# Kernel tuning notes

Hardware: AMD Instinct MI355X
Metric: run time of the kernel (lower is better)

Reference implementation:

```python
import jax, jax.numpy as jnp
import numpy as np

TEMPERATURE = 0.1
EPS = 1e-8


def setup_inputs() -> dict:
    key = jax.random.key(0)
    k1, k2 = jax.random.split(key)
    features = jax.random.normal(k1, (1024, 256, 16, 8), dtype=jnp.float32)
    labels = jax.random.randint(k2, (1024,), 0, 64, dtype=jnp.int64)
    return {"features": features, "labels": labels}


def reference(features, labels):
    B = features.shape[0]
    f = features.reshape(B, -1)
    norm = jnp.clip(jnp.linalg.norm(f, axis=1, keepdims=True), EPS)
    f = f / norm
    # matcher modeled as cosine-similarity gram matrix (opaque TransMatcher out of scope)
    scores = (f @ f.T) / TEMPERATURE  # [B, B]

    same = labels[:, None] == labels[None, :]
    eye = jnp.eye(B, dtype=bool)
    pos = same & ~eye  # positives excluding self
    neg = ~same & ~eye  # negatives excluding self

    # shared max over pos ∪ neg = all off-diagonal entries per row (matches original)
    row_max = jnp.max(jnp.where(eye, -jnp.inf, scores), axis=1, keepdims=True)
    e = jnp.exp(scores - row_max)  # [B, B]
    pos_sum = jnp.sum(jnp.where(pos, e, 0.0), axis=1)
    neg_sum = jnp.sum(jnp.where(neg, e, 0.0), axis=1)

    valid = jnp.any(pos, axis=1) & jnp.any(neg, axis=1)
    safe_pos = jnp.where(valid, pos_sum, 1.0)
    safe_neg = jnp.where(valid, neg_sum, 1.0)
    # loss_i = neg_term - pos_term; shared max cancels
    loss_i = jnp.where(valid, jnp.log(safe_neg) - jnp.log(safe_pos), 0.0)

    total = jnp.sum(valid.astype(jnp.float32))
    loss = jnp.where(total > 0, jnp.sum(loss_i) / jnp.maximum(total, 1.0), 0.0)

    max_pos = jnp.max(jnp.where(pos, scores, -jnp.inf), axis=1)
    max_neg = jnp.max(jnp.where(neg, scores, -jnp.inf), axis=1)
    correct = jnp.sum((valid & (max_pos > max_neg)).astype(jnp.float32))
    accuracy = jnp.where(total > 0, correct / jnp.maximum(total, 1.0), 0.5)
    return loss, accuracy
```

## Files before the change

### kernel.cpp

```cpp
#include <hip/hip_runtime.h>
#include <hip/hip_bf16.h>
#include <stdint.h>

#define BSZ 1024
#define KF 32768
#define SPLITK 32
#define KPER (KF / SPLITK)
#define BKB 128
#define TEMP_INV 10.0f

typedef float f32x4 __attribute__((ext_vector_type(4)));
typedef int v8i __attribute__((ext_vector_type(8)));

__device__ __forceinline__ void async_copy16(const void* g, void* l) {
    __builtin_amdgcn_global_load_lds(
        (const __attribute__((address_space(1))) void*)g,
        (__attribute__((address_space(3))) void*)l, 16, 0, 0);
}

__device__ __forceinline__ unsigned short f2bf_bits(float x) {
    union { float f; uint32_t u; } t; t.f = x;
    uint32_t r = t.u + 0x7FFFu + ((t.u >> 16) & 1u);
    return (unsigned short)(r >> 16);
}
__device__ __forceinline__ float bf2f(unsigned short b) {
    union { uint32_t u; float f; } t; t.u = ((uint32_t)b) << 16; return t.f;
}

__device__ __forceinline__ float waveSum(float v) {
    for (int o = 32; o > 0; o >>= 1) v += __shfl_down(v, o);
    return v;
}
__device__ __forceinline__ float waveMax(float v) {
    for (int o = 32; o > 0; o >>= 1) v = fmaxf(v, __shfl_down(v, o));
    return v;
}
__device__ __forceinline__ float blockSum(float v, float* red, int tid) {
    v = waveSum(v);
    __syncthreads();
    if ((tid & 63) == 0) red[tid >> 6] = v;
    __syncthreads();
    return red[0] + red[1] + red[2] + red[3];
}
__device__ __forceinline__ float blockMax(float v, float* red, int tid) {
    v = waveMax(v);
    __syncthreads();
    if ((tid & 63) == 0) red[tid >> 6] = v;
    __syncthreads();
    return fmaxf(fmaxf(red[0], red[1]), fmaxf(red[2], red[3]));
}

__global__ __launch_bounds__(256) void k_norm_convert(
    const float* __restrict__ f, unsigned char* __restrict__ f8,
    float* __restrict__ inv_norm) {
    int row = blockIdx.x, tid = threadIdx.x;
    const float4* src = (const float4*)(f + (size_t)row * KF);
    int4* dst = (int4*)(f8 + (size_t)row * KF);
    float ss = 0.f;
    for (int o = 0; o < 8; ++o) {
        int base4 = o * 1024 + tid * 4;
        int4 pk;
        int* pkp = &pk.x;
#pragma unroll
        for (int q = 0; q < 4; ++q) {
            float4 v = src[base4 + q];
            ss += v.x * v.x + v.y * v.y + v.z * v.z + v.w * v.w;
            int wd = __builtin_amdgcn_cvt_pk_fp8_f32(v.x, v.y, 0, false);
            wd = __builtin_amdgcn_cvt_pk_fp8_f32(v.z, v.w, wd, true);
            pkp[q] = wd;
        }
        dst[o * 256 + tid] = pk;
    }
    __shared__ float red[4];
    float tot = blockSum(ss, red, tid);
    if (tid == 0) inv_norm[row] = 1.0f / fmaxf(sqrtf(tot), 1e-8f);
}

__global__ __launch_bounds__(256) void k_gemm(
    const unsigned char* __restrict__ f8, unsigned short* __restrict__ partials) {
    __shared__ unsigned char Alds[128 * BKB];
    __shared__ unsigned char Blds[128 * BKB];
    int tid = threadIdx.x;

    int t = blockIdx.x;
    int bi = 0, accu = 0;
    while (accu + bi + 1 <= t) { accu += bi + 1; ++bi; }
    int bj = t - accu;
    int row0 = bi * 128, col0 = bj * 128;
    int p = blockIdx.y;
    size_t kbase = (size_t)p * KPER;

    const unsigned char* Ag = f8 + (size_t)row0 * KF;
    const unsigned char* Bg = f8 + (size_t)col0 * KF;
    int lane = tid & 63, w = tid >> 6;
    int wrow = (w >> 1) * 64, wcol = (w & 1) * 64;
    int mrow = lane & 15, quad = lane >> 4;

    int r_st[4], g_st[4];
#pragma unroll
    for (int c = 0; c < 4; ++c) {
        int idx = c * 256 + tid;
        r_st[c] = idx >> 3;
        g_st[c] = (idx & 7) ^ (r_st[c] & 7);
    }

    f32x4 acc[4][4] = {};

    for (int kt = 0; kt < KPER / BKB; ++kt) {
        size_t k0 = kbase + (size_t)kt * BKB;
        __syncthreads();
#pragma unroll
        for (int c = 0; c < 4; ++c) {
            int idx = c * 256 + tid;
            async_copy16(Ag + (size_t)r_st[c] * KF + k0 + g_st[c] * 16, &Alds[idx * 16]);
            async_copy16(Bg + (size_t)r_st[c] * KF + k0 + g_st[c] * 16, &Blds[idx * 16]);
        }
        __syncthreads();
        v8i a8[4], b8[4];
#pragma unroll
        for (int mi = 0; mi < 4; ++mi) {
            int rA = wrow + mi * 16 + mrow;
            int4 lo = *(const int4*)&Alds[rA * BKB + ((quad * 2)     ^ (rA & 7)) * 16];
            int4 hi = *(const int4*)&Alds[rA * BKB + ((quad * 2 + 1) ^ (rA & 7)) * 16];
            a8[mi] = (v8i){lo.x, lo.y, lo.z, lo.w, hi.x, hi.y, hi.z, hi.w};
        }
#pragma unroll
        for (int ni = 0; ni < 4; ++ni) {
            int rB = wcol + ni * 16 + mrow;
            int4 lo = *(const int4*)&Blds[rB * BKB + ((quad * 2)     ^ (rB & 7)) * 16];
            int4 hi = *(const int4*)&Blds[rB * BKB + ((quad * 2 + 1) ^ (rB & 7)) * 16];
            b8[ni] = (v8i){lo.x, lo.y, lo.z, lo.w, hi.x, hi.y, hi.z, hi.w};
        }
#pragma unroll
        for (int mi = 0; mi < 4; ++mi)
#pragma unroll
            for (int ni = 0; ni < 4; ++ni)
                acc[mi][ni] = __builtin_amdgcn_mfma_scale_f32_16x16x128_f8f6f4(
                    a8[mi], b8[ni], acc[mi][ni],
                    0, 0,
                    0, 0x7F7F7F7F,
                    0, 0x7F7F7F7F);
    }

    unsigned short* outp = partials + (size_t)p * BSZ * BSZ;
#pragma unroll
    for (int mi = 0; mi < 4; ++mi)
#pragma unroll
        for (int ni = 0; ni < 4; ++ni)
#pragma unroll
            for (int r = 0; r < 4; ++r) {
                int row = row0 + wrow + mi * 16 + quad * 4 + r;
                int col = col0 + wcol + ni * 16 + mrow;
                outp[(size_t)row * BSZ + col] = f2bf_bits(acc[mi][ni][r]);
            }
    if (bi != bj) {
#pragma unroll
        for (int mi = 0; mi < 4; ++mi)
#pragma unroll
            for (int ni = 0; ni < 4; ++ni) {
                int rowm = col0 + wcol + ni * 16 + mrow;
                int colm = row0 + wrow + mi * 16 + quad * 4;
                ushort4 v;
                v.x = f2bf_bits(acc[mi][ni][0]);
                v.y = f2bf_bits(acc[mi][ni][1]);
                v.z = f2bf_bits(acc[mi][ni][2]);
                v.w = f2bf_bits(acc[mi][ni][3]);
                *(ushort4*)&outp[(size_t)rowm * BSZ + colm] = v;
            }
    }
}

__global__ __launch_bounds__(256) void k_loss_rows(
    const unsigned short* __restrict__ partials, const float* __restrict__ inv_norm,
    const int* __restrict__ labels, float* __restrict__ rloss,
    float* __restrict__ rvalid, float* __restrict__ rcorr) {
    int i = blockIdx.x, tid = threadIdx.x;
    __shared__ float srow[BSZ];
    __shared__ int slab[BSZ];
    __shared__ float red[4];
    for (int c = 0; c < 4; ++c) slab[c * 256 + tid] = labels[c * 256 + tid];
    float inv_i = inv_norm[i];

    int j4 = tid * 4;
    float sx = 0.f, sy = 0.f, sz = 0.f, sw = 0.f;
#pragma unroll
    for (int p2 = 0; p2 < SPLITK; ++p2) {
        ushort4 v = *(const ushort4*)&partials[(size_t)p2 * BSZ * BSZ + (size_t)i * BSZ + j4];
        sx += bf2f(v.x); sy += bf2f(v.y); sz += bf2f(v.z); sw += bf2f(v.w);
    }
    float4 invj = *(const float4*)&inv_norm[j4];
    srow[j4 + 0] = sx * inv_i * invj.x * TEMP_INV;
    srow[j4 + 1] = sy * inv_i * invj.y * TEMP_INV;
    srow[j4 + 2] = sz * inv_i * invj.z * TEMP_INV;
    srow[j4 + 3] = sw * inv_i * invj.w * TEMP_INV;
    __syncthreads();

    int lab_i = slab[i];
    float lm = -3.0e38f;
    for (int c = 0; c < 4; ++c) {
        int j = c * 256 + tid;
        if (j != i) lm = fmaxf(lm, srow[j]);
    }
    float rowmax = blockMax(lm, red, tid);

    float pos_sum = 0.f, neg_sum = 0.f, mp = -3.0e38f, mn = -3.0e38f;
    for (int c = 0; c < 4; ++c) {
        int j = c * 256 + tid;
        if (j == i) continue;
        float s = srow[j];
        float e = expf(s - rowmax);
        if (slab[j] == lab_i) { pos_sum += e; mp = fmaxf(mp, s); }
        else                  { neg_sum += e; mn = fmaxf(mn, s); }
    }
    float ps = blockSum(pos_sum, red, tid);
    float ns = blockSum(neg_sum, red, tid);
    float mpa = blockMax(mp, red, tid);
    float mna = blockMax(mn, red, tid);
    if (tid == 0) {
        bool valid = (mpa > -1.0e37f) && (mna > -1.0e37f);
        rloss[i]  = valid ? (logf(ns) - logf(ps)) : 0.f;
        rvalid[i] = valid ? 1.f : 0.f;
        rcorr[i]  = (valid && (mpa > mna)) ? 1.f : 0.f;
    }
}

__global__ __launch_bounds__(256) void k_final(
    const float* __restrict__ rloss, const float* __restrict__ rvalid,
    const float* __restrict__ rcorr, float* __restrict__ out) {
    __shared__ float red[4];
    int tid = threadIdx.x;
    float sl = 0.f, sv = 0.f, sc = 0.f;
    for (int c = 0; c < 4; ++c) {
        int j = c * 256 + tid;
        sl += rloss[j]; sv += rvalid[j]; sc += rcorr[j];
    }
    sl = blockSum(sl, red, tid);
    sv = blockSum(sv, red, tid);
    sc = blockSum(sc, red, tid);
    if (tid == 0) {
        out[0] = (sv > 0.f) ? sl / fmaxf(sv, 1.f) : 0.f;
        out[1] = (sv > 0.f) ? sc / fmaxf(sv, 1.f) : 0.5f;
    }
}

extern "C" void kernel_launch(void* const* d_in, const int* in_sizes, int n_in,
                              void* d_out, int out_size, void* d_ws, size_t ws_size,
                              hipStream_t stream) {
    const float* feats = (const float*)d_in[0];
    const int* labels = (const int*)d_in[1];
    float* out = (float*)d_out;
    char* ws = (char*)d_ws;

    unsigned char* f8        = (unsigned char*)ws;
    unsigned short* partials = (unsigned short*)(ws + (size_t)32 * 1024 * 1024);
    float* inv_norm          = (float*)(ws + (size_t)96 * 1024 * 1024);
    float* rloss             = inv_norm + BSZ;
    float* rvalid            = rloss + BSZ;
    float* rcorr             = rvalid + BSZ;

    k_norm_convert<<<BSZ, 256, 0, stream>>>(feats, f8, inv_norm);
    k_gemm<<<dim3(36, SPLITK), 256, 0, stream>>>(f8, partials);
    k_loss_rows<<<BSZ, 256, 0, stream>>>(partials, inv_norm, labels, rloss, rvalid, rcorr);
    k_final<<<1, 256, 0, stream>>>(rloss, rvalid, rcorr, out);
}
```

Baseline: 263.7 us.

## Store split-K partials in fp8, use fixed exp shift, fuse final reduction via atomics

Split-K partial sums of the Gram matrix are now stored as fp8 instead of bf16, which halves the partial buffer traffic written by the GEMM and read by the loss kernel. The per-row max pass is removed by using a constant shift of 10 (the maximum possible cosine score over the temperature), and the exp call becomes the fast intrinsic. The final reduction kernel is folded into the loss kernel through global atomics and a last-block ticket. In exchange, fp8 partials lose a lot of precision across 32 accumulated slices, the fixed shift could underflow for rows whose scores are all far below 10, and float atomics make the summation order nondeterministic.

```diff
diff --git a/kernel.cpp b/kernel.cpp
--- a/kernel.cpp
+++ b/kernel.cpp
@@ -18,15 +18,6 @@
         (__attribute__((address_space(3))) void*)l, 16, 0, 0);
 }
 
-__device__ __forceinline__ unsigned short f2bf_bits(float x) {
-    union { float f; uint32_t u; } t; t.f = x;
-    uint32_t r = t.u + 0x7FFFu + ((t.u >> 16) & 1u);
-    return (unsigned short)(r >> 16);
-}
-__device__ __forceinline__ float bf2f(unsigned short b) {
-    union { uint32_t u; float f; } t; t.u = ((uint32_t)b) << 16; return t.f;
-}
-
 __device__ __forceinline__ float waveSum(float v) {
     for (int o = 32; o > 0; o >>= 1) v += __shfl_down(v, o);
     return v;
@@ -52,8 +43,9 @@
 
 __global__ __launch_bounds__(256) void k_norm_convert(
     const float* __restrict__ f, unsigned char* __restrict__ f8,
-    float* __restrict__ inv_norm) {
+    float* __restrict__ inv_norm, float* __restrict__ gaccum) {
     int row = blockIdx.x, tid = threadIdx.x;
+    if (row == 0 && tid < 4) gaccum[tid] = 0.f;
     const float4* src = (const float4*)(f + (size_t)row * KF);
     int4* dst = (int4*)(f8 + (size_t)row * KF);
     float ss = 0.f;
@@ -77,7 +69,7 @@
 }
 
 __global__ __launch_bounds__(256) void k_gemm(
-    const unsigned char* __restrict__ f8, unsigned short* __restrict__ partials) {
+    const unsigned char* __restrict__ f8, unsigned char* __restrict__ partials) {
     __shared__ unsigned char Alds[128 * BKB];
     __shared__ unsigned char Blds[128 * BKB];
     int tid = threadIdx.x;
@@ -142,7 +134,7 @@
                     0, 0x7F7F7F7F);
     }
 
-    unsigned short* outp = partials + (size_t)p * BSZ * BSZ;
+    unsigned char* outp = partials + (size_t)p * BSZ * BSZ;
 #pragma unroll
     for (int mi = 0; mi < 4; ++mi)
 #pragma unroll
@@ -151,7 +143,9 @@
             for (int r = 0; r < 4; ++r) {
                 int row = row0 + wrow + mi * 16 + quad * 4 + r;
                 int col = col0 + wcol + ni * 16 + mrow;
-                outp[(size_t)row * BSZ + col] = f2bf_bits(acc[mi][ni][r]);
+                int b = __builtin_amdgcn_cvt_pk_fp8_f32(
+                            acc[mi][ni][r], acc[mi][ni][r], 0, false);
+                outp[(size_t)row * BSZ + col] = (unsigned char)(b & 0xFF);
             }
     if (bi != bj) {
 #pragma unroll
@@ -160,24 +154,23 @@
             for (int ni = 0; ni < 4; ++ni) {
                 int rowm = col0 + wcol + ni * 16 + mrow;
                 int colm = row0 + wrow + mi * 16 + quad * 4;
-                ushort4 v;
-                v.x = f2bf_bits(acc[mi][ni][0]);
-                v.y = f2bf_bits(acc[mi][ni][1]);
-                v.z = f2bf_bits(acc[mi][ni][2]);
-                v.w = f2bf_bits(acc[mi][ni][3]);
-                *(ushort4*)&outp[(size_t)rowm * BSZ + colm] = v;
+                int pk = __builtin_amdgcn_cvt_pk_fp8_f32(
+                             acc[mi][ni][0], acc[mi][ni][1], 0, false);
+                pk = __builtin_amdgcn_cvt_pk_fp8_f32(
+                         acc[mi][ni][2], acc[mi][ni][3], pk, true);
+                *(int*)&outp[(size_t)rowm * BSZ + colm] = pk;
             }
     }
 }
 
 __global__ __launch_bounds__(256) void k_loss_rows(
-    const unsigned short* __restrict__ partials, const float* __restrict__ inv_norm,
-    const int* __restrict__ labels, float* __restrict__ rloss,
-    float* __restrict__ rvalid, float* __restrict__ rcorr) {
+    const unsigned char* __restrict__ partials, const float* __restrict__ inv_norm,
+    const int* __restrict__ labels, float* __restrict__ gaccum,
+    float* __restrict__ out) {
     int i = blockIdx.x, tid = threadIdx.x;
-    __shared__ float srow[BSZ];
     __shared__ int slab[BSZ];
     __shared__ float red[4];
+    __shared__ int s_ticket;
     for (int c = 0; c < 4; ++c) slab[c * 256 + tid] = labels[c * 256 + tid];
     float inv_i = inv_norm[i];
 
@@ -185,30 +178,28 @@
     float sx = 0.f, sy = 0.f, sz = 0.f, sw = 0.f;
 #pragma unroll
     for (int p2 = 0; p2 < SPLITK; ++p2) {
-        ushort4 v = *(const ushort4*)&partials[(size_t)p2 * BSZ * BSZ + (size_t)i * BSZ + j4];
-        sx += bf2f(v.x); sy += bf2f(v.y); sz += bf2f(v.z); sw += bf2f(v.w);
+        int v = *(const int*)&partials[(size_t)p2 * BSZ * BSZ + (size_t)i * BSZ + j4];
+        sx += __builtin_amdgcn_cvt_f32_fp8(v, 0);
+        sy += __builtin_amdgcn_cvt_f32_fp8(v, 1);
+        sz += __builtin_amdgcn_cvt_f32_fp8(v, 2);
+        sw += __builtin_amdgcn_cvt_f32_fp8(v, 3);
     }
     float4 invj = *(const float4*)&inv_norm[j4];
-    srow[j4 + 0] = sx * inv_i * invj.x * TEMP_INV;
-    srow[j4 + 1] = sy * inv_i * invj.y * TEMP_INV;
-    srow[j4 + 2] = sz * inv_i * invj.z * TEMP_INV;
-    srow[j4 + 3] = sw * inv_i * invj.w * TEMP_INV;
+    float s4[4];
+    s4[0] = sx * inv_i * invj.x * TEMP_INV;
+    s4[1] = sy * inv_i * invj.y * TEMP_INV;
+    s4[2] = sz * inv_i * invj.z * TEMP_INV;
+    s4[3] = sw * inv_i * invj.w * TEMP_INV;
     __syncthreads();
 
     int lab_i = slab[i];
-    float lm = -3.0e38f;
-    for (int c = 0; c < 4; ++c) {
-        int j = c * 256 + tid;
-        if (j != i) lm = fmaxf(lm, srow[j]);
-    }
-    float rowmax = blockMax(lm, red, tid);
-
     float pos_sum = 0.f, neg_sum = 0.f, mp = -3.0e38f, mn = -3.0e38f;
-    for (int c = 0; c < 4; ++c) {
-        int j = c * 256 + tid;
+#pragma unroll
+    for (int q = 0; q < 4; ++q) {
+        int j = j4 + q;
         if (j == i) continue;
-        float s = srow[j];
-        float e = expf(s - rowmax);
+        float s = s4[q];
+        float e = __expf(s - 10.0f);
         if (slab[j] == lab_i) { pos_sum += e; mp = fmaxf(mp, s); }
         else                  { neg_sum += e; mn = fmaxf(mn, s); }
     }
@@ -216,28 +207,21 @@
     float ns = blockSum(neg_sum, red, tid);
     float mpa = blockMax(mp, red, tid);
     float mna = blockMax(mn, red, tid);
+
     if (tid == 0) {
         bool valid = (mpa > -1.0e37f) && (mna > -1.0e37f);
-        rloss[i]  = valid ? (logf(ns) - logf(ps)) : 0.f;
-        rvalid[i] = valid ? 1.f : 0.f;
-        rcorr[i]  = (valid && (mpa > mna)) ? 1.f : 0.f;
-    }
-}
-
-__global__ __launch_bounds__(256) void k_final(
-    const float* __restrict__ rloss, const float* __restrict__ rvalid,
-    const float* __restrict__ rcorr, float* __restrict__ out) {
-    __shared__ float red[4];
-    int tid = threadIdx.x;
-    float sl = 0.f, sv = 0.f, sc = 0.f;
-    for (int c = 0; c < 4; ++c) {
-        int j = c * 256 + tid;
-        sl += rloss[j]; sv += rvalid[j]; sc += rcorr[j];
-    }
-    sl = blockSum(sl, red, tid);
-    sv = blockSum(sv, red, tid);
-    sc = blockSum(sc, red, tid);
-    if (tid == 0) {
+        float li = valid ? (logf(ns) - logf(ps)) : 0.f;
+        atomicAdd(&gaccum[0], li);
+        atomicAdd(&gaccum[1], valid ? 1.f : 0.f);
+        atomicAdd(&gaccum[2], (valid && (mpa > mna)) ? 1.f : 0.f);
+        __threadfence();
+        s_ticket = atomicAdd((int*)&gaccum[3], 1);
+    }
+    __syncthreads();
+    if (s_ticket == BSZ - 1 && tid == 0) {
+        float sl = atomicAdd(&gaccum[0], 0.f);
+        float sv = atomicAdd(&gaccum[1], 0.f);
+        float sc = atomicAdd(&gaccum[2], 0.f);
         out[0] = (sv > 0.f) ? sl / fmaxf(sv, 1.f) : 0.f;
         out[1] = (sv > 0.f) ? sc / fmaxf(sv, 1.f) : 0.5f;
     }
@@ -251,15 +235,12 @@
     float* out = (float*)d_out;
     char* ws = (char*)d_ws;
 
-    unsigned char* f8        = (unsigned char*)ws;
-    unsigned short* partials = (unsigned short*)(ws + (size_t)32 * 1024 * 1024);
-    float* inv_norm          = (float*)(ws + (size_t)96 * 1024 * 1024);
-    float* rloss             = inv_norm + BSZ;
-    float* rvalid            = rloss + BSZ;
-    float* rcorr             = rvalid + BSZ;
-
-    k_norm_convert<<<BSZ, 256, 0, stream>>>(feats, f8, inv_norm);
+    unsigned char* f8       = (unsigned char*)ws;
+    unsigned char* partials = (unsigned char*)(ws + (size_t)32 * 1024 * 1024);
+    float* inv_norm         = (float*)(ws + (size_t)64 * 1024 * 1024);
+    float* gaccum           = inv_norm + BSZ;
+
+    k_norm_convert<<<BSZ, 256, 0, stream>>>(feats, f8, inv_norm, gaccum);
     k_gemm<<<dim3(36, SPLITK), 256, 0, stream>>>(f8, partials);
-    k_loss_rows<<<BSZ, 256, 0, stream>>>(partials, inv_norm, labels, rloss, rvalid, rcorr);
-    k_final<<<1, 256, 0, stream>>>(rloss, rvalid, rcorr, out);
-}
+    k_loss_rows<<<BSZ, 256, 0, stream>>>(partials, inv_norm, labels, gaccum, out);
+}
```

Result: slower. 300.7 us (+14.0%).
